# Optimization experiments

Hardware: AMD Instinct MI355X
Metric: run time of the kernel (lower is better)

Reference implementation:

```python
import math
import jax, jax.numpy as jnp
import numpy as np

D_MODEL = 1024
NUM_HEADS = 16
D_HEAD = D_MODEL // NUM_HEADS  # 64
K_S = 32  # sparse top-k keys kept per query
B, N = 2, 2048


def setup_inputs() -> dict:
    key = jax.random.key(0)
    ks = jax.random.split(key, 9)
    s = 1.0 / math.sqrt(D_MODEL)
    return {
        "x": jax.random.normal(ks[0], (B, N, D_MODEL), dtype=jnp.float32),
        "Wq": jax.random.normal(ks[1], (D_MODEL, D_MODEL), dtype=jnp.float32) * s,
        "bq": jnp.zeros((D_MODEL,), dtype=jnp.float32),
        "Wk": jax.random.normal(ks[2], (D_MODEL, D_MODEL), dtype=jnp.float32) * s,
        "bk": jnp.zeros((D_MODEL,), dtype=jnp.float32),
        "Wv": jax.random.normal(ks[3], (D_MODEL, D_MODEL), dtype=jnp.float32) * s,
        "bv": jnp.zeros((D_MODEL,), dtype=jnp.float32),
        "Wo": jax.random.normal(ks[4], (D_MODEL, D_MODEL), dtype=jnp.float32) * s,
        "bo": jnp.zeros((D_MODEL,), dtype=jnp.float32),
    }


def _attn(x, Wq, bq, Wk, bk, Wv, bv, Wo, bo):
    b, n, _ = x.shape
    # projections (torch Linear: y = x W^T + b)
    q = (x @ Wq.T + bq).reshape(b, n, NUM_HEADS, D_HEAD).transpose(0, 2, 1, 3)
    k = (x @ Wk.T + bk).reshape(b, n, NUM_HEADS, D_HEAD).transpose(0, 2, 1, 3)
    v = (x @ Wv.T + bv).reshape(b, n, NUM_HEADS, D_HEAD).transpose(0, 2, 1, 3)
    # full scores [b, H, n, n]
    scores = jnp.einsum("bhqd,bhkd->bhqk", q, k) / math.sqrt(D_HEAD)
    # causal mask (triu above diagonal -> -inf)
    causal = jnp.triu(jnp.ones((n, n), dtype=bool), k=1)
    neg_inf = jnp.array(-jnp.inf, dtype=scores.dtype)
    scores = jnp.where(causal, neg_inf, scores)
    # sparse top-k: keep only K_S largest scores per query row
    vals, idx = jax.lax.top_k(scores, K_S)
    masked = jnp.full_like(scores, -jnp.inf)
    masked = jnp.put_along_axis(masked, idx, vals, axis=-1, inplace=False)
    attn = jax.nn.softmax(masked, axis=-1)  # dropout p=0.0 -> identity
    out = jnp.einsum("bhqk,bhkd->bhqd", attn, v)
    out = out.transpose(0, 2, 1, 3).reshape(b, n, D_MODEL)
    y = out @ Wo.T + bo
    return y, attn.mean(axis=1)


def reference(x, Wq, bq, Wk, bk, Wv, bv, Wo, bo):
    return _attn(x, Wq, bq, Wk, bk, Wv, bv, Wo, bo)
```

## Files before the change

### kernel.cpp

```cpp
#include <hip/hip_runtime.h>
#include <hip/hip_bf16.h>
#include <math.h>

#define BATCH   2
#define NTOK    2048
#define DMODEL  1024
#define HEADS   16
#define DHEAD   64
#define KSEL    32
#define MROWS   (BATCH * NTOK)
#define NBLK8   (NTOK / 8)
#define TPW     4

typedef short     bf16x8 __attribute__((ext_vector_type(8)));
typedef float     f32x4  __attribute__((ext_vector_type(4)));
typedef unsigned short ushort_t;
typedef unsigned long long u64;

#define GLOAD_LDS16(g, l) \
    __builtin_amdgcn_global_load_lds((const __attribute__((address_space(1))) void*)(g), \
                                     (__attribute__((address_space(3))) void*)(l), 16, 0, 0)

__device__ __forceinline__ ushort_t f2bf(float f) {
    unsigned u = __float_as_uint(f);
    unsigned r = (u + 0x7FFFu + ((u >> 16) & 1u)) >> 16;
    return (ushort_t)r;
}
__device__ __forceinline__ float bf2f(ushort_t h) {
    return __uint_as_float(((unsigned)h) << 16);
}

__device__ __forceinline__ void conv_body(const float* __restrict__ in,
                                          ushort_t* __restrict__ hi,
                                          ushort_t* __restrict__ lo, int n, int i)
{
    if (i + 3 < n) {
        const float4 v = *(const float4*)(in + i);
        ushort4 ph, pl;
        ph.x = f2bf(v.x); pl.x = f2bf(v.x - bf2f(ph.x));
        ph.y = f2bf(v.y); pl.y = f2bf(v.y - bf2f(ph.y));
        ph.z = f2bf(v.z); pl.z = f2bf(v.z - bf2f(ph.z));
        ph.w = f2bf(v.w); pl.w = f2bf(v.w - bf2f(ph.w));
        *(ushort4*)(hi + i) = ph;
        *(ushort4*)(lo + i) = pl;
    }
}

__global__ __launch_bounds__(256) void conv_split(const float* __restrict__ in,
                                                  ushort_t* __restrict__ hi,
                                                  ushort_t* __restrict__ lo, int n)
{
    const int i = (blockIdx.x * 256 + threadIdx.x) * 4;
    conv_body(in, hi, lo, n, i);
}

__global__ __launch_bounds__(256) void conv_split4(const float* __restrict__ i0, ushort_t* __restrict__ h0, ushort_t* __restrict__ l0,
                                                   const float* __restrict__ i1, ushort_t* __restrict__ h1, ushort_t* __restrict__ l1,
                                                   const float* __restrict__ i2, ushort_t* __restrict__ h2, ushort_t* __restrict__ l2,
                                                   const float* __restrict__ i3, ushort_t* __restrict__ h3, ushort_t* __restrict__ l3,
                                                   int n)
{
    const int w = blockIdx.y;
    const float* in = (w == 0) ? i0 : (w == 1) ? i1 : (w == 2) ? i2 : i3;
    ushort_t* hi = (w == 0) ? h0 : (w == 1) ? h1 : (w == 2) ? h2 : h3;
    ushort_t* lo = (w == 0) ? l0 : (w == 1) ? l1 : (w == 2) ? l2 : l3;
    const int i = (blockIdx.x * 256 + threadIdx.x) * 4;
    conv_body(in, hi, lo, n, i);
}

__global__ __launch_bounds__(256) void zero_fill(float* __restrict__ p, int n4)
{
    const int i = blockIdx.x * 256 + threadIdx.x;
    if (i < n4) ((float4*)p)[i] = (float4){0.f, 0.f, 0.f, 0.f};
}

__device__ __forceinline__ unsigned mono_key(float f) {
    const unsigned u = __float_as_uint(f);
    return (u ^ (unsigned)(((int)u >> 31) | 0x80000000)) + 1u;
}
__device__ __forceinline__ float unmono(unsigned m) {
    const unsigned u = m - 1u;
    return __uint_as_float(u ^ (unsigned)(((int)(~u) >> 31) | 0x80000000));
}

__device__ __forceinline__ void xcd_tile_map(int* m0, int* n0)
{
    const int lin = blockIdx.x + (blockIdx.y << 5);
    const int xcd = lin & 7;
    const int s   = lin >> 3;
    *m0 = (xcd * 4 + (s >> 4)) * 128;
    *n0 = (s & 15) * 64;
}

__global__ __launch_bounds__(256, 2) void gemm_qkv_fused(const ushort_t* __restrict__ xhi,
                                                         const ushort_t* __restrict__ xlo,
                                                         const ushort_t* __restrict__ wqh,
                                                         const ushort_t* __restrict__ wql,
                                                         const ushort_t* __restrict__ wkh,
                                                         const ushort_t* __restrict__ wkl,
                                                         const ushort_t* __restrict__ wvh,
                                                         const ushort_t* __restrict__ wvl,
                                                         const float* __restrict__ bq,
                                                         const float* __restrict__ bk,
                                                         const float* __restrict__ bv,
                                                         ushort_t* __restrict__ Qh,
                                                         ushort_t* __restrict__ Qm,
                                                         ushort_t* __restrict__ Ql,
                                                         ushort_t* __restrict__ Kh,
                                                         ushort_t* __restrict__ Km,
                                                         ushort_t* __restrict__ Kl,
                                                         float* __restrict__ Vws)
{
    __shared__ ushort_t smem[2 * 20480];

    const int tid  = threadIdx.x;
    const int wave = tid >> 6;
    const int lane = tid & 63;
    const int fr   = lane & 15;
    const int k8   = lane >> 4;
    int m0, n0;
    xcd_tile_map(&m0, &n0);

    f32x4 acc[3][2][4];
#pragma unroll
    for (int w = 0; w < 3; ++w)
#pragma unroll
        for (int i = 0; i < 2; ++i)
#pragma unroll
            for (int j = 0; j < 4; ++j) acc[w][i][j] = (f32x4){0.f, 0.f, 0.f, 0.f};

#define STAGEF(bufsel, k0v) do {                                               \
        ushort_t* dst_ = smem + (size_t)(bufsel) * 20480;                      \
        _Pragma("unroll")                                                      \
        for (int i_ = 0; i_ < 2; ++i_) {                                       \
            const int c_ = i_ * 256 + tid;                                     \
            const int row_ = c_ >> 2;                                          \
            const int g_ = (c_ & 3) ^ ((row_ >> 1) & 3);                       \
            const size_t ga_ = (size_t)(m0 + row_) * DMODEL + (k0v) + g_ * 8;  \
            GLOAD_LDS16(xhi + ga_, dst_ + (size_t)c_ * 8);                     \
            GLOAD_LDS16(xlo + ga_, dst_ + 4096 + (size_t)c_ * 8);              \
        }                                                                      \
        {                                                                      \
            const int c_ = tid;                                                \
            const int row_ = c_ >> 2;                                          \
            const int g_ = (c_ & 3) ^ ((row_ >> 1) & 3);                       \
            const size_t gb_ = (size_t)(n0 + row_) * DMODEL + (k0v) + g_ * 8;  \
            GLOAD_LDS16(wqh + gb_, dst_ + 8192 + (size_t)c_ * 8);              \
            GLOAD_LDS16(wql + gb_, dst_ + 10240 + (size_t)c_ * 8);             \
            GLOAD_LDS16(wkh + gb_, dst_ + 12288 + (size_t)c_ * 8);             \
            GLOAD_LDS16(wkl + gb_, dst_ + 14336 + (size_t)c_ * 8);             \
            GLOAD_LDS16(wvh + gb_, dst_ + 16384 + (size_t)c_ * 8);             \
            GLOAD_LDS16(wvl + gb_, dst_ + 18432 + (size_t)c_ * 8);             \
        }                                                                      \
    } while (0)

    STAGEF(0, 0);
    int cur = 0;

    for (int k0 = 0; k0 < DMODEL; k0 += 32) {
        __syncthreads();
        if (k0 + 32 < DMODEL) STAGEF(cur ^ 1, k0 + 32);

        const ushort_t* buf = smem + (size_t)cur * 20480;
        bf16x8 afh[2], afl[2];
#pragma unroll
        for (int mi = 0; mi < 2; ++mi) {
            const int r = wave * 32 + mi * 16 + fr;
            const int ro = r * 32 + (k8 ^ ((r >> 1) & 3)) * 8;
            afh[mi] = *(const bf16x8*)(buf + ro);
            afl[mi] = *(const bf16x8*)(buf + 4096 + ro);
        }

#pragma unroll
        for (int w = 0; w < 3; ++w) {
            const ushort_t* bb = buf + 8192 + w * 4096;
            bf16x8 bfh[4], bfl[4];
#pragma unroll
            for (int ni = 0; ni < 4; ++ni) {
                const int r = ni * 16 + fr;
                const int ro = r * 32 + (k8 ^ ((r >> 1) & 3)) * 8;
                bfh[ni] = *(const bf16x8*)(bb + ro);
                bfl[ni] = *(const bf16x8*)(bb + 2048 + ro);
            }
#pragma unroll
            for (int mi = 0; mi < 2; ++mi)
#pragma unroll
                for (int ni = 0; ni < 4; ++ni) {
                    acc[w][mi][ni] = __builtin_amdgcn_mfma_f32_16x16x32_bf16(afh[mi], bfl[ni], acc[w][mi][ni], 0, 0, 0);
                    acc[w][mi][ni] = __builtin_amdgcn_mfma_f32_16x16x32_bf16(afl[mi], bfh[ni], acc[w][mi][ni], 0, 0, 0);
                    acc[w][mi][ni] = __builtin_amdgcn_mfma_f32_16x16x32_bf16(afh[mi], bfh[ni], acc[w][mi][ni], 0, 0, 0);
                }
        }
        cur ^= 1;
    }
#undef STAGEF

#pragma unroll
    for (int w = 0; w < 3; ++w) {
        const float* bias = (w == 0) ? bq : (w == 1) ? bk : bv;
        ushort_t* oh = (w == 0) ? Qh : Kh;
        ushort_t* om = (w == 0) ? Qm : Km;
        ushort_t* ol = (w == 0) ? Ql : Kl;
#pragma unroll
        for (int ni = 0; ni < 4; ++ni) {
            const int o = n0 + ni * 16 + (lane & 15);
            const float bvv = bias[o];
            const int hd = o >> 6;
            const int d  = o & 63;
#pragma unroll
            for (int mi = 0; mi < 2; ++mi) {
#pragma unroll
                for (int reg = 0; reg < 4; ++reg) {
                    const int m = m0 + wave * 32 + mi * 16 + ((lane >> 4) << 2) + reg;
                    const float v = acc[w][mi][ni][reg] + bvv;
                    const int bb = m >> 11;
                    const int n  = m & 2047;
                    const size_t off = (((size_t)(bb * HEADS + hd)) * NTOK + n) * DHEAD + d;
                    if (w == 2) {
                        Vws[off] = v;
                    } else {
                        const ushort_t h1 = f2bf(v);
                        const float r1 = v - bf2f(h1);
                        const ushort_t m1 = f2bf(r1);
                        const ushort_t l1 = f2bf(r1 - bf2f(m1));
                        oh[off] = h1; om[off] = m1; ol[off] = l1;
                    }
                }
            }
        }
    }
}

__global__ __launch_bounds__(256, 2) void gemm_split_mfma(const ushort_t* __restrict__ Ahi,
                                                          const ushort_t* __restrict__ Alo,
                                                          const ushort_t* __restrict__ Bhi,
                                                          const ushort_t* __restrict__ Blo,
                                                          const float* __restrict__ bias,
                                                          float* __restrict__ out)
{
    __shared__ ushort_t smem[2 * 12288];

    const int tid  = threadIdx.x;
    const int wave = tid >> 6;
    const int lane = tid & 63;
    const int fr   = lane & 15;
    const int k8   = lane >> 4;
    int m0, n0;
    xcd_tile_map(&m0, &n0);

    f32x4 acc[2][4];
#pragma unroll
    for (int i = 0; i < 2; ++i)
#pragma unroll
        for (int j = 0; j < 4; ++j) acc[i][j] = (f32x4){0.f, 0.f, 0.f, 0.f};

#define STAGE(bufsel, k0v) do {                                                \
        ushort_t* dst_ = smem + (size_t)(bufsel) * 12288;                      \
        _Pragma("unroll")                                                      \
        for (int i_ = 0; i_ < 2; ++i_) {                                       \
            const int c_ = i_ * 256 + tid;                                     \
            const int row_ = c_ >> 2;                                          \
            const int g_ = (c_ & 3) ^ ((row_ >> 1) & 3);                       \
            const size_t ga_ = (size_t)(m0 + row_) * DMODEL + (k0v) + g_ * 8;  \
            GLOAD_LDS16(Ahi + ga_, dst_ + (size_t)c_ * 8);                     \
            GLOAD_LDS16(Alo + ga_, dst_ + 4096 + (size_t)c_ * 8);              \
        }                                                                      \
        {                                                                      \
            const int c_ = tid;                                                \
            const int row_ = c_ >> 2;                                          \
            const int g_ = (c_ & 3) ^ ((row_ >> 1) & 3);                       \
            const size_t gb_ = (size_t)(n0 + row_) * DMODEL + (k0v) + g_ * 8;  \
            GLOAD_LDS16(Bhi + gb_, dst_ + 8192 + (size_t)c_ * 8);              \
            GLOAD_LDS16(Blo + gb_, dst_ + 10240 + (size_t)c_ * 8);             \
        }                                                                      \
    } while (0)

    STAGE(0, 0);
    int cur = 0;

    for (int k0 = 0; k0 < DMODEL; k0 += 32) {
        __syncthreads();
        if (k0 + 32 < DMODEL) STAGE(cur ^ 1, k0 + 32);

        const ushort_t* buf = smem + (size_t)cur * 12288;
        bf16x8 afh[2], afl[2], bfh[4], bfl[4];
#pragma unroll
        for (int mi = 0; mi < 2; ++mi) {
            const int r = wave * 32 + mi * 16 + fr;
            const int ro = r * 32 + (k8 ^ ((r >> 1) & 3)) * 8;
            afh[mi] = *(const bf16x8*)(buf + ro);
            afl[mi] = *(const bf16x8*)(buf + 4096 + ro);
        }
#pragma unroll
        for (int ni = 0; ni < 4; ++ni) {
            const int r = ni * 16 + fr;
            const int ro = r * 32 + (k8 ^ ((r >> 1) & 3)) * 8;
            bfh[ni] = *(const bf16x8*)(buf + 8192 + ro);
            bfl[ni] = *(const bf16x8*)(buf + 10240 + ro);
        }

#pragma unroll
        for (int mi = 0; mi < 2; ++mi)
#pragma unroll
            for (int ni = 0; ni < 4; ++ni) {
                acc[mi][ni] = __builtin_amdgcn_mfma_f32_16x16x32_bf16(afh[mi], bfl[ni], acc[mi][ni], 0, 0, 0);
                acc[mi][ni] = __builtin_amdgcn_mfma_f32_16x16x32_bf16(afl[mi], bfh[ni], acc[mi][ni], 0, 0, 0);
                acc[mi][ni] = __builtin_amdgcn_mfma_f32_16x16x32_bf16(afh[mi], bfh[ni], acc[mi][ni], 0, 0, 0);
            }
        cur ^= 1;
    }
#undef STAGE

#pragma unroll
    for (int ni = 0; ni < 4; ++ni) {
        const int o = n0 + ni * 16 + (lane & 15);
        const float bv = bias[o];
#pragma unroll
        for (int mi = 0; mi < 2; ++mi) {
#pragma unroll
            for (int reg = 0; reg < 4; ++reg) {
                const int m = m0 + wave * 32 + mi * 16 + ((lane >> 4) << 2) + reg;
                out[(size_t)m * DMODEL + o] = acc[mi][ni][reg] + bv;
            }
        }
    }
}

__global__ __launch_bounds__(256, 3) void score_mfma(const ushort_t* __restrict__ Qh,
                                                     const ushort_t* __restrict__ Qm,
                                                     const ushort_t* __restrict__ Ql,
                                                     const ushort_t* __restrict__ Kh,
                                                     const ushort_t* __restrict__ Km,
                                                     const ushort_t* __restrict__ Kl,
                                                     unsigned* __restrict__ S,
                                                     unsigned* __restrict__ Smax,
                                                     int q0, int QC)
{
    const int ks = blockIdx.x;
    const int qt = blockIdx.y;
    const int bh = blockIdx.z;
    const int qbase = q0 + qt * 128;
    const int ktmax = ((qbase + 127) >> 6) + 1;
    const int kt0 = ks * TPW;
    if (kt0 >= ktmax) return;
    const int kt1 = (kt0 + TPW < ktmax) ? (kt0 + TPW) : ktmax;

    __shared__ ushort_t smem[2 * 12288];

    const int tid  = threadIdx.x;
    const int wave = tid >> 6;
    const int lane = tid & 63;
    const int l15  = lane & 15;
    const int l4   = lane >> 4;

    const size_t qgbase = ((size_t)bh * NTOK + qbase) * DHEAD;

    bf16x8 qf[3][2][2];
#pragma unroll
    for (int p = 0; p < 3; ++p) {
        const ushort_t* Qp = (p == 0) ? Qh : (p == 1) ? Qm : Ql;
#pragma unroll
        for (int j = 0; j < 2; ++j) {
            const int r = wave * 32 + j * 16 + l15;
#pragma unroll
            for (int h = 0; h < 2; ++h)
                qf[p][j][h] = *(const bf16x8*)(Qp + qgbase + (size_t)r * DHEAD + (h * 4 + l4) * 8);
        }
    }

#define STAGE_K(bufsel, ktv) do {                                              \
        const size_t kg_ = ((size_t)bh * NTOK + (ktv) * 64) * DHEAD;           \
        _Pragma("unroll")                                                      \
        for (int i_ = 0; i_ < 2; ++i_) {                                       \
            const int c_ = i_ * 256 + tid;                                     \
            const int row_ = c_ >> 3;                                          \
            const int g_ = (c_ & 7) ^ (row_ & 7);                              \
            const size_t goff_ = kg_ + (size_t)row_ * DHEAD + g_ * 8;          \
            ushort_t* dst_ = smem + (bufsel) * 12288 + (size_t)c_ * 8;         \
            GLOAD_LDS16(Kh + goff_, dst_ + 0 * 4096);                          \
            GLOAD_LDS16(Km + goff_, dst_ + 1 * 4096);                          \
            GLOAD_LDS16(Kl + goff_, dst_ + 2 * 4096);                          \
        }                                                                      \
    } while (0)

    STAGE_K(0, kt0);
    __builtin_amdgcn_sched_barrier(0);
    asm volatile("s_waitcnt vmcnt(0)" ::: "memory");
    __builtin_amdgcn_s_barrier();
    __builtin_amdgcn_sched_barrier(0);

    int cur = 0;
    const size_t srowQ = (size_t)bh * QC;

    for (int kt = kt0; kt < kt1; ++kt) {
        const bool more = (kt + 1 < kt1);
        if (more) STAGE_K(cur ^ 1, kt + 1);
        __builtin_amdgcn_sched_barrier(0);

        f32x4 acc[4][2];
#pragma unroll
        for (int m = 0; m < 4; ++m)
#pragma unroll
            for (int j = 0; j < 2; ++j) acc[m][j] = (f32x4){0.f, 0.f, 0.f, 0.f};

        const ushort_t* kb = smem + cur * 12288;
#pragma unroll
        for (int h = 0; h < 2; ++h) {
            bf16x8 kf[4];
#pragma unroll
            for (int m = 0; m < 4; ++m) {
                const int r = m * 16 + l15;
                const int slot = (h * 4 + l4) ^ (r & 7);
                kf[m] = *(const bf16x8*)(kb + 0 * 4096 + (size_t)(r * 8 + slot) * 8);
            }
#pragma unroll
            for (int m = 0; m < 4; ++m)
#pragma unroll
                for (int j = 0; j < 2; ++j) {
                    acc[m][j] = __builtin_amdgcn_mfma_f32_16x16x32_bf16(kf[m], qf[2][j][h], acc[m][j], 0, 0, 0);
                    acc[m][j] = __builtin_amdgcn_mfma_f32_16x16x32_bf16(kf[m], qf[1][j][h], acc[m][j], 0, 0, 0);
                    acc[m][j] = __builtin_amdgcn_mfma_f32_16x16x32_bf16(kf[m], qf[0][j][h], acc[m][j], 0, 0, 0);
                }
#pragma unroll
            for (int m = 0; m < 4; ++m) {
                const int r = m * 16 + l15;
                const int slot = (h * 4 + l4) ^ (r & 7);
                kf[m] = *(const bf16x8*)(kb + 1 * 4096 + (size_t)(r * 8 + slot) * 8);
            }
#pragma unroll
            for (int m = 0; m < 4; ++m)
#pragma unroll
                for (int j = 0; j < 2; ++j) {
                    acc[m][j] = __builtin_amdgcn_mfma_f32_16x16x32_bf16(kf[m], qf[1][j][h], acc[m][j], 0, 0, 0);
                    acc[m][j] = __builtin_amdgcn_mfma_f32_16x16x32_bf16(kf[m], qf[0][j][h], acc[m][j], 0, 0, 0);
                }
#pragma unroll
            for (int m = 0; m < 4; ++m) {
                const int r = m * 16 + l15;
                const int slot = (h * 4 + l4) ^ (r & 7);
                kf[m] = *(const bf16x8*)(kb + 2 * 4096 + (size_t)(r * 8 + slot) * 8);
            }
#pragma unroll
            for (int m = 0; m < 4; ++m)
#pragma unroll
                for (int j = 0; j < 2; ++j)
                    acc[m][j] = __builtin_amdgcn_mfma_f32_16x16x32_bf16(kf[m], qf[0][j][h], acc[m][j], 0, 0, 0);
        }

#pragma unroll
        for (int j = 0; j < 2; ++j) {
            const int qrow  = wave * 32 + j * 16 + l15;
            const int qlrow = qt * 128 + qrow;
            const int qglob = qbase + qrow;
            const size_t srow = (srowQ + qlrow) * NTOK;
            const size_t mrow = (srowQ + qlrow) * NBLK8;
#pragma unroll
            for (int m = 0; m < 4; ++m) {
                const int kcol0 = kt * 64 + m * 16 + (l4 << 2);
                uint4 kv;
                kv.x = mono_key(acc[m][j][0] * 0.125f);
                kv.y = mono_key(acc[m][j][1] * 0.125f);
                kv.z = mono_key(acc[m][j][2] * 0.125f);
                kv.w = mono_key(acc[m][j][3] * 0.125f);
                *(uint4*)(S + srow + kcol0) = kv;
                unsigned cm = (kcol0     <= qglob) ? kv.x : 0u;
                unsigned t;
                t = (kcol0 + 1 <= qglob) ? kv.y : 0u; cm = (t > cm) ? t : cm;
                t = (kcol0 + 2 <= qglob) ? kv.z : 0u; cm = (t > cm) ? t : cm;
                t = (kcol0 + 3 <= qglob) ? kv.w : 0u; cm = (t > cm) ? t : cm;
                const unsigned o = __shfl_xor(cm, 16, 64);
                cm = (o > cm) ? o : cm;
                if ((lane & 16) == 0) {
                    const int gblk = kt * 8 + m * 2 + (lane >> 5);
                    Smax[mrow + gblk] = cm;
                }
            }
        }

        if (more) {
            asm volatile("s_waitcnt vmcnt(16)" ::: "memory");
            __builtin_amdgcn_s_barrier();
            __builtin_amdgcn_sched_barrier(0);
        }
        cur ^= 1;
    }
#undef STAGE_K
}

__global__ __launch_bounds__(256) void select_v7(const unsigned* __restrict__ S,
                                                 const unsigned* __restrict__ Smax,
                                                 const float* __restrict__ V,
                                                 float* __restrict__ ctx,
                                                 float* __restrict__ attn,
                                                 int q0, int QC)
{
    __shared__ int   sBlkAll[4][KSEL];
    __shared__ int   sIdxAll[4][KSEL];
    __shared__ float sEAll[4][KSEL];

    const int lane = threadIdx.x & 63;
    const int wave = threadIdx.x >> 6;
    const int ql = blockIdx.x;
    const int b  = blockIdx.y >> 2;
    const int hg = blockIdx.y & 3;
    const int h  = hg * 4 + wave;
    const int q  = q0 + ql;
    const int L  = q + 1;
    const int nsel = (L < KSEL) ? L : KSEL;
    const int nb = (L + 7) >> 3;

    const size_t bhx = (size_t)(b * HEADS + h);
    const unsigned* Srow = S + (bhx * QC + ql) * NTOK;
    const unsigned* Mrow = Smax + (bhx * QC + ql) * NBLK8;
    const float* Vb   = V + bhx * NTOK * DHEAD;
    float* ctxRow  = ctx + (((size_t)(b * NTOK + q)) * HEADS + h) * DHEAD;
    float* attnRow = attn + ((size_t)(b * NTOK + q)) * NTOK;
    int*   sBlk = sBlkAll[wave];
    int*   sIdx = sIdxAll[wave];
    float* sE   = sEAll[wave];

    const uint4 bm4 = *(const uint4*)(Mrow + lane * 4);
    unsigned bmax[4] = {bm4.x, bm4.y, bm4.z, bm4.w};
#pragma unroll
    for (int s = 0; s < 4; ++s)
        if (lane * 4 + s >= nb) bmax[s] = 0u;

    unsigned gmax = bmax[0];
    gmax = (bmax[1] > gmax) ? bmax[1] : gmax;
    gmax = (bmax[2] > gmax) ? bmax[2] : gmax;
    gmax = (bmax[3] > gmax) ? bmax[3] : gmax;
#pragma unroll
    for (int d = 1; d < 64; d <<= 1) {
        const unsigned o = __shfl_xor(gmax, d, 64);
        gmax = (o > gmax) ? o : gmax;
    }
    const float vmax = unmono(gmax);

    unsigned selb = 0u;
    unsigned blkLo = 1u;
    int nselb;
    if (nb <= KSEL) {
        nselb = nb;
#pragma unroll
        for (int s = 0; s < 4; ++s)
            if (lane * 4 + s < nb) selb |= 1u << s;
    } else {
        nselb = KSEL;
        unsigned lo = 1u, hi = gmax >> 16;
        while (lo < hi) {
            const unsigned mid = lo + ((hi - lo + 1u) >> 1);
            const unsigned midk = mid << 16;
            int cnt = 0;
#pragma unroll
            for (int s = 0; s < 4; ++s)
                cnt += __popcll(__ballot(bmax[s] >= midk));
            if (cnt >= KSEL) lo = mid; else hi = mid - 1u;
        }
        blkLo = lo;
        const unsigned Tkb = lo << 16;
        const unsigned Gkb = Tkb | 0xFFFFu;
        int cge = 0, cgt = 0;
#pragma unroll
        for (int s = 0; s < 4; ++s) {
            cge += __popcll(__ballot(bmax[s] >= Tkb));
            cgt += __popcll(__ballot(bmax[s] > Gkb));
        }
        if (cge == KSEL) {
#pragma unroll
            for (int s = 0; s < 4; ++s)
                selb |= (bmax[s] >= Tkb) ? (1u << s) : 0u;
        } else {
            unsigned bmb = 0u;
#pragma unroll
            for (int s = 0; s < 4; ++s) {
                selb |= (bmax[s] > Gkb) ? (1u << s) : 0u;
                bmb  |= (bmax[s] >= Tkb && bmax[s] <= Gkb) ? (1u << s) : 0u;
            }
            int k_tie = KSEL - cgt;
            while (k_tie > 0) {
                u64 best = 0;
                unsigned bmm = bmb;
                while (bmm) {
                    const int s = __builtin_ctz(bmm);
                    bmm &= bmm - 1u;
                    const unsigned gblk = (unsigned)(lane * 4 + s);
                    const u64 k = ((u64)bmax[s] << 32) | (unsigned)~gblk;
                    if (k > best) best = k;
                }
                u64 bb = best;
#pragma unroll
                for (int d = 1; d < 64; d <<= 1) {
                    const u64 o = __shfl_xor(bb, d, 64);
                    bb = (o > bb) ? o : bb;
                }
                const unsigned gblk = ~(unsigned)bb;
                if (lane == (int)(gblk >> 2)) {
                    const unsigned bit = 1u << (gblk & 3u);
                    selb |= bit;
                    bmb &= ~bit;
                }
                --k_tie;
            }
        }
    }

    {
        const int cb = __popc(selb);
        int pfxb = cb;
#pragma unroll
        for (int d = 1; d < 64; d <<= 1) {
            const int t = __shfl_up(pfxb, d, 64);
            if (lane >= d) pfxb += t;
        }
        pfxb -= cb;
        unsigned mskb = selb;
        int posb = pfxb;
        while (mskb) {
            const int s = __builtin_ctz(mskb);
            mskb &= mskb - 1u;
            sBlk[posb++] = lane * 4 + s;
        }
    }
    __asm volatile("s_waitcnt lgkmcnt(0)" ::: "memory");

    const int NC = nselb * 8;
    unsigned km[4];
    int idx[4];
#pragma unroll
    for (int c = 0; c < 4; ++c) {
        const int t = c * 64 + lane;
        unsigned m = 0u;
        int j = 0;
        if (t < NC) {
            const int blk = sBlk[t >> 3];
            j = blk * 8 + (t & 7);
            if (j < L) m = Srow[j];
        }
        km[c] = m;
        idx[c] = j;
    }

    unsigned lo = blkLo, hi = gmax >> 16;
    while (lo < hi) {
        const unsigned mid = lo + ((hi - lo + 1u) >> 1);
        const unsigned midk = mid << 16;
        int cnt = 0;
#pragma unroll
        for (int c = 0; c < 4; ++c)
            cnt += __popcll(__ballot(km[c] >= midk));
        if (cnt >= nsel) lo = mid; else hi = mid - 1u;
    }
    const unsigned Tk = lo << 16;
    const unsigned Gk = Tk | 0xFFFFu;

    int cnt_ge = 0, cnt_gt = 0;
#pragma unroll
    for (int c = 0; c < 4; ++c) {
        cnt_ge += __popcll(__ballot(km[c] >= Tk));
        cnt_gt += __popcll(__ballot(km[c] > Gk));
    }

    unsigned selmask = 0u;
    if (cnt_ge == nsel) {
#pragma unroll
        for (int c = 0; c < 4; ++c)
            selmask |= (km[c] >= Tk) ? (1u << c) : 0u;
    } else {
        unsigned bmask = 0u;
#pragma unroll
        for (int c = 0; c < 4; ++c) {
            selmask |= (km[c] > Gk) ? (1u << c) : 0u;
            bmask   |= (km[c] >= Tk && km[c] <= Gk) ? (1u << c) : 0u;
        }
        int k_tie = nsel - cnt_gt;
        while (k_tie > 0) {
            u64 best = 0;
            unsigned bmm = bmask;
            while (bmm) {
                const int c = __builtin_ctz(bmm);
                bmm &= bmm - 1u;
                const int t = c * 64 + lane;
                const u64 k = ((u64)km[c] << 32) |
                              ((u64)(0xFFFFu ^ (unsigned)idx[c]) << 16) | (u64)t;
                if (k > best) best = k;
            }
            u64 bb = best;
#pragma unroll
            for (int d = 1; d < 64; d <<= 1) {
                const u64 o = __shfl_xor(bb, d, 64);
                bb = (o > bb) ? o : bb;
            }
            const unsigned tt = (unsigned)bb & 0xFFFFu;
            if (lane == (int)(tt & 63u)) {
                const unsigned bit = 1u << (tt >> 6);
                selmask |= bit;
                bmask &= ~bit;
            }
            --k_tie;
        }
    }

    const int csel = __popc(selmask);
    int pfx = csel;
#pragma unroll
    for (int d = 1; d < 64; d <<= 1) {
        const int t = __shfl_up(pfx, d, 64);
        if (lane >= d) pfx += t;
    }
    pfx -= csel;

    float esum = 0.f;
    unsigned msk = selmask;
    int pos = pfx;
    while (msk) {
        const int c = __builtin_ctz(msk);
        msk &= msk - 1u;
        const float e = __expf(unmono(km[c]) - vmax);
        esum += e;
        sIdx[pos] = idx[c];
        sE[pos] = e;
        ++pos;
    }

    float Z = esum;
#pragma unroll
    for (int d = 1; d < 64; d <<= 1) Z += __shfl_xor(Z, d, 64);
    const float rcpZ = 1.0f / Z;

    msk = selmask;
    pos = pfx;
    while (msk) {
        const int c = __builtin_ctz(msk);
        msk &= msk - 1u;
        const float w = sE[pos] * rcpZ;
        ++pos;
        atomicAdd(&attnRow[idx[c]], w * (1.0f / (float)HEADS));
    }

    {
        float a0 = 0.f, a1 = 0.f, a2 = 0.f, a3 = 0.f;
        int i = 0;
#pragma unroll 2
        for (; i + 4 <= nsel; i += 4) {
            const int i0 = sIdx[i],     i1 = sIdx[i + 1];
            const int i2 = sIdx[i + 2], i3 = sIdx[i + 3];
            const float w0 = sE[i]     * rcpZ, w1 = sE[i + 1] * rcpZ;
            const float w2 = sE[i + 2] * rcpZ, w3 = sE[i + 3] * rcpZ;
            a0 += w0 * Vb[(size_t)i0 * DHEAD + lane];
            a1 += w1 * Vb[(size_t)i1 * DHEAD + lane];
            a2 += w2 * Vb[(size_t)i2 * DHEAD + lane];
            a3 += w3 * Vb[(size_t)i3 * DHEAD + lane];
        }
        for (; i < nsel; ++i)
            a0 += sE[i] * rcpZ * Vb[(size_t)sIdx[i] * DHEAD + lane];
        ctxRow[lane] = (a0 + a1) + (a2 + a3);
    }
}

extern "C" void kernel_launch(void* const* d_in, const int* in_sizes, int n_in,
                              void* d_out, int out_size, void* d_ws, size_t ws_size,
                              hipStream_t stream) {
    const float* x  = (const float*)d_in[0];
    const float* Wq = (const float*)d_in[1];
    const float* bq = (const float*)d_in[2];
    const float* Wk = (const float*)d_in[3];
    const float* bk = (const float*)d_in[4];
    const float* Wv = (const float*)d_in[5];
    const float* bv = (const float*)d_in[6];
    const float* Wo = (const float*)d_in[7];
    const float* bo = (const float*)d_in[8];

    const size_t MB = 1ull << 20;
    char* wsb = (char*)d_ws;
    float*    Vws = (float*)(wsb + 0 * MB);
    float*    ctx = (float*)(wsb + 16 * MB);
    ushort_t* xhi = (ushort_t*)(wsb + 32 * MB);
    ushort_t* xlo = (ushort_t*)(wsb + 40 * MB);
    ushort_t* wqh = (ushort_t*)(wsb + 48 * MB);
    ushort_t* wql = (ushort_t*)(wsb + 50 * MB);
    ushort_t* wkh = (ushort_t*)(wsb + 52 * MB);
    ushort_t* wkl = (ushort_t*)(wsb + 54 * MB);
    ushort_t* wvh = (ushort_t*)(wsb + 56 * MB);
    ushort_t* wvl = (ushort_t*)(wsb + 58 * MB);
    ushort_t* woh = (ushort_t*)(wsb + 60 * MB);
    ushort_t* wol = (ushort_t*)(wsb + 62 * MB);
    ushort_t* Qh  = (ushort_t*)(wsb + 64 * MB);
    ushort_t* Qm  = (ushort_t*)(wsb + 72 * MB);
    ushort_t* Ql  = (ushort_t*)(wsb + 80 * MB);
    ushort_t* Kh  = (ushort_t*)(wsb + 88 * MB);
    ushort_t* Km  = (ushort_t*)(wsb + 96 * MB);
    ushort_t* Kl  = (ushort_t*)(wsb + 104 * MB);
    ushort_t* cxh = xhi;
    ushort_t* cxl = xlo;

    float* y    = (float*)d_out;
    float* attn = y + (size_t)BATCH * NTOK * DMODEL;

    const int NX = MROWS * DMODEL;
    const int NW = DMODEL * DMODEL;

    conv_split<<<NX / (256 * 4), 256, 0, stream>>>(x, xhi, xlo, NX);
    {
        dim3 cgrid(NW / (256 * 4), 4);
        conv_split4<<<cgrid, 256, 0, stream>>>(Wq, wqh, wql,
                                               Wk, wkh, wkl,
                                               Wv, wvh, wvl,
                                               Wo, woh, wol, NW);
    }

    dim3 ggrid(MROWS / 128, DMODEL / 64);
    gemm_qkv_fused<<<ggrid, 256, 0, stream>>>(xhi, xlo,
                                              wqh, wql, wkh, wkl, wvh, wvl,
                                              bq, bk, bv,
                                              Qh, Qm, Ql, Kh, Km, Kl, Vws);

    const size_t base_bytes = 112 * MB;
    const size_t avail = (ws_size > base_bytes) ? ws_size - base_bytes : 0;
    int QC = 128;
    for (int cand = 512; cand >= 128; cand >>= 1) {
        const size_t need = (size_t)BATCH * HEADS * cand * (size_t)(NTOK + NBLK8) * sizeof(unsigned);
        if (need <= avail) { QC = cand; break; }
    }
    unsigned* Smax = (unsigned*)(wsb + base_bytes);
    unsigned* Sws  = (unsigned*)(wsb + base_bytes +
                                 (size_t)BATCH * HEADS * QC * NBLK8 * sizeof(unsigned));

    const int nattn4 = BATCH * NTOK * NTOK / 4;
    zero_fill<<<(nattn4 + 255) / 256, 256, 0, stream>>>(attn, nattn4);
    for (int q0 = 0; q0 < NTOK; q0 += QC) {
        const int ktm = (q0 + QC) >> 6;
        dim3 sgrid((ktm + TPW - 1) / TPW, QC / 128, BATCH * HEADS);
        score_mfma<<<sgrid, 256, 0, stream>>>(Qh, Qm, Ql, Kh, Km, Kl, Sws, Smax, q0, QC);
        dim3 selgrid(QC, BATCH * 4);
        select_v7<<<selgrid, 256, 0, stream>>>(Sws, Smax, Vws, ctx, attn, q0, QC);
    }

    conv_split<<<NX / (256 * 4), 256, 0, stream>>>(ctx, cxh, cxl, NX);
    gemm_split_mfma<<<ggrid, 256, 0, stream>>>(cxh, cxl, woh, wol, bo, y);
}
```

Measured before the change: 505.8 us.

## Accumulate head-averaged attention in LDS per row and drop global zero-fill

The select kernel now processes all 16 heads of one (batch, query) row in a single block. Head-mean attention weights are accumulated in a shared-memory row, then written once to global memory with vector stores. This removes the separate zero-fill pass over the 32 MB attention output and replaces global atomics with LDS atomics. It also drops the XCD-aware tile remapping in both GEMMs in favour of a plain blockIdx mapping, which may hurt L2 locality. The select grid is 4x smaller, so each block runs four sequential heads per wave.

```diff
diff --git a/kernel.cpp b/kernel.cpp
--- a/kernel.cpp
+++ b/kernel.cpp
@@ -68,12 +68,6 @@
     conv_body(in, hi, lo, n, i);
 }
 
-__global__ __launch_bounds__(256) void zero_fill(float* __restrict__ p, int n4)
-{
-    const int i = blockIdx.x * 256 + threadIdx.x;
-    if (i < n4) ((float4*)p)[i] = (float4){0.f, 0.f, 0.f, 0.f};
-}
-
 __device__ __forceinline__ unsigned mono_key(float f) {
     const unsigned u = __float_as_uint(f);
     return (u ^ (unsigned)(((int)u >> 31) | 0x80000000)) + 1u;
@@ -81,15 +75,6 @@
 __device__ __forceinline__ float unmono(unsigned m) {
     const unsigned u = m - 1u;
     return __uint_as_float(u ^ (unsigned)(((int)(~u) >> 31) | 0x80000000));
-}
-
-__device__ __forceinline__ void xcd_tile_map(int* m0, int* n0)
-{
-    const int lin = blockIdx.x + (blockIdx.y << 5);
-    const int xcd = lin & 7;
-    const int s   = lin >> 3;
-    *m0 = (xcd * 4 + (s >> 4)) * 128;
-    *n0 = (s & 15) * 64;
 }
 
 __global__ __launch_bounds__(256, 2) void gemm_qkv_fused(const ushort_t* __restrict__ xhi,
@@ -118,8 +103,8 @@
     const int lane = tid & 63;
     const int fr   = lane & 15;
     const int k8   = lane >> 4;
-    int m0, n0;
-    xcd_tile_map(&m0, &n0);
+    const int m0 = blockIdx.x * 128;
+    const int n0 = blockIdx.y * 64;
 
     f32x4 acc[3][2][4];
 #pragma unroll
@@ -245,8 +230,8 @@
     const int lane = tid & 63;
     const int fr   = lane & 15;
     const int k8   = lane >> 4;
-    int m0, n0;
-    xcd_tile_map(&m0, &n0);
+    const int m0 = blockIdx.x * 128;
+    const int n0 = blockIdx.y * 64;
 
     f32x4 acc[2][4];
 #pragma unroll
@@ -487,38 +472,17 @@
 #undef STAGE_K
 }
 
-__global__ __launch_bounds__(256) void select_v7(const unsigned* __restrict__ S,
-                                                 const unsigned* __restrict__ Smax,
-                                                 const float* __restrict__ V,
-                                                 float* __restrict__ ctx,
-                                                 float* __restrict__ attn,
-                                                 int q0, int QC)
+__device__ __forceinline__ void select_task8(const unsigned* __restrict__ Srow,
+                                             const unsigned* __restrict__ Mrow,
+                                             const float* __restrict__ Vb,
+                                             float* __restrict__ ctxRow,
+                                             float* __restrict__ attnS,
+                                             int L, int nsel, int nb,
+                                             int* __restrict__ sBlk,
+                                             int* __restrict__ sIdx,
+                                             float* __restrict__ sE,
+                                             int lane)
 {
-    __shared__ int   sBlkAll[4][KSEL];
-    __shared__ int   sIdxAll[4][KSEL];
-    __shared__ float sEAll[4][KSEL];
-
-    const int lane = threadIdx.x & 63;
-    const int wave = threadIdx.x >> 6;
-    const int ql = blockIdx.x;
-    const int b  = blockIdx.y >> 2;
-    const int hg = blockIdx.y & 3;
-    const int h  = hg * 4 + wave;
-    const int q  = q0 + ql;
-    const int L  = q + 1;
-    const int nsel = (L < KSEL) ? L : KSEL;
-    const int nb = (L + 7) >> 3;
-
-    const size_t bhx = (size_t)(b * HEADS + h);
-    const unsigned* Srow = S + (bhx * QC + ql) * NTOK;
-    const unsigned* Mrow = Smax + (bhx * QC + ql) * NBLK8;
-    const float* Vb   = V + bhx * NTOK * DHEAD;
-    float* ctxRow  = ctx + (((size_t)(b * NTOK + q)) * HEADS + h) * DHEAD;
-    float* attnRow = attn + ((size_t)(b * NTOK + q)) * NTOK;
-    int*   sBlk = sBlkAll[wave];
-    int*   sIdx = sIdxAll[wave];
-    float* sE   = sEAll[wave];
-
     const uint4 bm4 = *(const uint4*)(Mrow + lane * 4);
     unsigned bmax[4] = {bm4.x, bm4.y, bm4.z, bm4.w};
 #pragma unroll
@@ -734,7 +698,7 @@
         msk &= msk - 1u;
         const float w = sE[pos] * rcpZ;
         ++pos;
-        atomicAdd(&attnRow[idx[c]], w * (1.0f / (float)HEADS));
+        atomicAdd(&attnS[idx[c]], w * (1.0f / (float)HEADS));
     }
 
     {
@@ -754,6 +718,58 @@
         for (; i < nsel; ++i)
             a0 += sE[i] * rcpZ * Vb[(size_t)sIdx[i] * DHEAD + lane];
         ctxRow[lane] = (a0 + a1) + (a2 + a3);
+    }
+}
+
+__global__ __launch_bounds__(256) void select_v8(const unsigned* __restrict__ S,
+                                                 const unsigned* __restrict__ Smax,
+                                                 const float* __restrict__ V,
+                                                 float* __restrict__ ctx,
+                                                 float* __restrict__ attn,
+                                                 int q0, int QC)
+{
+    __shared__ float attnS[NTOK];
+    __shared__ int   sBlkAll[4][KSEL];
+    __shared__ int   sIdxAll[4][KSEL];
+    __shared__ float sEAll[4][KSEL];
+
+    const int lane = threadIdx.x & 63;
+    const int wave = threadIdx.x >> 6;
+    const int ql = blockIdx.x;
+    const int b  = blockIdx.y;
+    const int q  = q0 + ql;
+    const int L  = q + 1;
+    const int nsel = (L < KSEL) ? L : KSEL;
+    const int nb = (L + 7) >> 3;
+
+    {
+        float4* a4 = (float4*)attnS;
+#pragma unroll
+        for (int i = 0; i < NTOK / 4 / 256; ++i)
+            a4[i * 256 + threadIdx.x] = (float4){0.f, 0.f, 0.f, 0.f};
+    }
+    __syncthreads();
+
+#pragma unroll
+    for (int hi = 0; hi < 4; ++hi) {
+        const int h = hi * 4 + wave;
+        const size_t bhx = (size_t)(b * HEADS + h);
+        const unsigned* Srow = S + (bhx * QC + ql) * NTOK;
+        const unsigned* Mrow = Smax + (bhx * QC + ql) * NBLK8;
+        const float* Vb = V + bhx * NTOK * DHEAD;
+        float* ctxRow = ctx + (((size_t)(b * NTOK + q)) * HEADS + h) * DHEAD;
+        select_task8(Srow, Mrow, Vb, ctxRow, attnS, L, nsel, nb,
+                     sBlkAll[wave], sIdxAll[wave], sEAll[wave], lane);
+    }
+    __syncthreads();
+
+    {
+        float* attnRow = attn + ((size_t)(b * NTOK + q)) * NTOK;
+        const float4* a4 = (const float4*)attnS;
+        float4* o4 = (float4*)attnRow;
+#pragma unroll
+        for (int i = 0; i < NTOK / 4 / 256; ++i)
+            o4[i * 256 + threadIdx.x] = a4[i * 256 + threadIdx.x];
     }
 }
 
@@ -825,14 +841,12 @@
     unsigned* Sws  = (unsigned*)(wsb + base_bytes +
                                  (size_t)BATCH * HEADS * QC * NBLK8 * sizeof(unsigned));
 
-    const int nattn4 = BATCH * NTOK * NTOK / 4;
-    zero_fill<<<(nattn4 + 255) / 256, 256, 0, stream>>>(attn, nattn4);
     for (int q0 = 0; q0 < NTOK; q0 += QC) {
         const int ktm = (q0 + QC) >> 6;
         dim3 sgrid((ktm + TPW - 1) / TPW, QC / 128, BATCH * HEADS);
         score_mfma<<<sgrid, 256, 0, stream>>>(Qh, Qm, Ql, Kh, Km, Kl, Sws, Smax, q0, QC);
-        dim3 selgrid(QC, BATCH * 4);
-        select_v7<<<selgrid, 256, 0, stream>>>(Sws, Smax, Vws, ctx, attn, q0, QC);
+        dim3 selgrid(QC, BATCH);
+        select_v8<<<selgrid, 256, 0, stream>>>(Sws, Smax, Vws, ctx, attn, q0, QC);
     }
 
     conv_split<<<NX / (256 * 4), 256, 0, stream>>>(ctx, cxh, cxl, NX);
```

Measured after the change: 505.3 us. No clear change (-0.1%).
